# Optimization experiments

Hardware: AMD Instinct MI355X
Metric: run time of the kernel (lower is better)

Reference implementation:

```python
import jax, jax.numpy as jnp
import numpy as np

N_NODES = 100000
N_EDGES = 3200000
IN_DIM = 128
OUT_DIM = 128


def setup_inputs() -> dict:
    key = jax.random.key(0)
    k1, k2, k3, k4, k5 = jax.random.split(key, 5)
    fea_input = jax.random.normal(k1, (N_NODES, IN_DIM), dtype=jnp.float32)
    edge_row = jax.random.randint(k2, (N_EDGES,), 0, N_NODES, dtype=jnp.int32)
    edge_col = jax.random.randint(k3, (N_EDGES,), 0, N_NODES, dtype=jnp.int32)
    edge_val = jax.random.uniform(k4, (N_EDGES,), dtype=jnp.float32)
    # kaiming_uniform-style init for weight, zeros for bias
    bound = float(np.sqrt(6.0 / IN_DIM))
    weight = jax.random.uniform(k5, (IN_DIM, OUT_DIM), dtype=jnp.float32,
                                minval=-bound, maxval=bound)
    bias = jnp.zeros((OUT_DIM,), dtype=jnp.float32)
    return {
        "fea_input": fea_input,
        "edge_row": edge_row,
        "edge_col": edge_col,
        "edge_val": edge_val,
        "weight": weight,
        "bias": bias,
    }


def reference(fea_input, edge_row, edge_col, edge_val, weight, bias):
    # support = X @ W  -> [N, OUT_DIM]
    support = jnp.matmul(fea_input, weight)
    # SpMM: out[r] += val * support[c] for each edge (r, c, val)
    gathered = support[edge_col] * edge_val[:, None]  # [E, OUT_DIM]
    output = jax.ops.segment_sum(gathered, edge_row, num_segments=N_NODES)
    return output + bias
```

## Files before the change

### kernel.cpp

```cpp
#include <hip/hip_runtime.h>
#include <hip/hip_bf16.h>


#define N_NODES 100000
#define N_EDGES 3200000
#define DIM 128
#define RB 16
#define RPB 128
#define NBKT ((N_NODES + RPB - 1) / RPB)
#define CHUNK 8192
#define NCHK ((N_EDGES + CHUNK - 1) / CHUNK)
#define CAP 6016

typedef __attribute__((ext_vector_type(8))) short bf16x8;
typedef __attribute__((ext_vector_type(4))) float f32x4;
typedef unsigned long long u64;
typedef unsigned int u32;

__device__ inline ushort bf16rne(float f) {
  uint32_t u = __float_as_uint(f);
  u += 0x7fffu + ((u >> 16) & 1u);
  return (ushort)(u >> 16);
}
__device__ inline float pk_val(u32 w) { return __uint_as_float((w & 0x7fffu) << 16); }
__device__ inline u32 pk_col(u32 w) { return w >> 15; }

__global__ __launch_bounds__(256) void prep_count_kernel(
    const float* __restrict__ X, const float* __restrict__ W,
    ushort* __restrict__ Xh, ushort* __restrict__ Wh,
    const int* __restrict__ erow, int* __restrict__ bcnt) {
  __shared__ int cnt[NBKT];
  if (blockIdx.x < 1024) {
    const size_t nx4 = (size_t)N_NODES * DIM / 4;
    const size_t nw4 = (size_t)DIM * DIM / 4;
    for (size_t i = (size_t)blockIdx.x * blockDim.x + threadIdx.x;
         i < nx4 + nw4; i += (size_t)1024 * blockDim.x) {
      const float4 f = (i < nx4) ? ((const float4*)X)[i] : ((const float4*)W)[i - nx4];
      ushort4 h;
      h.x = bf16rne(f.x); h.y = bf16rne(f.y); h.z = bf16rne(f.z); h.w = bf16rne(f.w);
      if (i < nx4) ((ushort4*)Xh)[i] = h;
      else         ((ushort4*)Wh)[i - nx4] = h;
    }
  } else {
    const int cb = blockIdx.x - 1024;
    for (int b = threadIdx.x; b < NBKT; b += 256) cnt[b] = 0;
    __syncthreads();
    const int e0 = cb * CHUNK;
    #pragma unroll
    for (int it = 0; it < CHUNK / 256; ++it) {
      const int e = e0 + it * 256 + threadIdx.x;
      if (e < N_EDGES) atomicAdd(&cnt[erow[e] >> 7], 1);
    }
    __syncthreads();
    for (int b = threadIdx.x; b < NBKT; b += 256) {
      const int c = cnt[b];
      if (c) atomicAdd(&bcnt[b], c);
    }
  }
}

__global__ __launch_bounds__(1024) void bscan_kernel(int* __restrict__ bcur,
                                                     int* __restrict__ bbase) {
  __shared__ int wsum[16];
  const int t = threadIdx.x, lane = t & 63, wid = t >> 6;
  const int v = (t < NBKT) ? bcur[t] : 0;
  int incl = v;
  #pragma unroll
  for (int off = 1; off < 64; off <<= 1) {
    int n = __shfl_up(incl, off, 64);
    if (lane >= off) incl += n;
  }
  if (lane == 63) wsum[wid] = incl;
  __syncthreads();
  if (t == 0) {
    int s = 0;
    #pragma unroll
    for (int w = 0; w < 16; ++w) { int x = wsum[w]; wsum[w] = s; s += x; }
  }
  __syncthreads();
  const int excl = wsum[wid] + incl - v;
  if (t < NBKT) { bbase[t] = excl; bcur[t] = excl; }
  if (t == NBKT - 1) bbase[NBKT] = excl + v;
}

__global__ __launch_bounds__(256) void partition_kernel(
    const int* __restrict__ erow, const int* __restrict__ ecol,
    const float* __restrict__ eval,
    int* __restrict__ bcur, u64* __restrict__ p64) {
  __shared__ int cnt[NBKT];
  const int e0 = blockIdx.x * CHUNK;
  for (int b = threadIdx.x; b < NBKT; b += 256) cnt[b] = 0;
  __syncthreads();
  #pragma unroll
  for (int it = 0; it < CHUNK / 256; ++it) {
    const int e = e0 + it * 256 + threadIdx.x;
    if (e < N_EDGES) atomicAdd(&cnt[erow[e] >> 7], 1);
  }
  __syncthreads();
  for (int b = threadIdx.x; b < NBKT; b += 256) {
    const int c = cnt[b];
    if (c) cnt[b] = atomicAdd(&bcur[b], c);
  }
  __syncthreads();
  #pragma unroll
  for (int it = 0; it < CHUNK / 256; ++it) {
    const int e = e0 + it * 256 + threadIdx.x;
    if (e < N_EDGES) {
      const int r = erow[e];
      const u32 lo = ((u32)ecol[e] << 15) | (u32)bf16rne(eval[e]);
      const int p = atomicAdd(&cnt[r >> 7], 1);
      p64[p] = ((u64)(r & (RPB - 1)) << 32) | (u64)lo;
    }
  }
}

__global__ __launch_bounds__(256) void bsort_kernel(
    const int* __restrict__ bbase, u64* __restrict__ p64,
    int* __restrict__ row_ptr, ushort* __restrict__ row_len) {
  __shared__ u64 ebuf[CAP];
  __shared__ u32 obuf[CAP];
  __shared__ int hist[RPB];
  __shared__ int excl[RPB];
  __shared__ int wtot;
  const int b = blockIdx.x, t = threadIdx.x;
  const int s = bbase[b];
  int nE = bbase[b + 1] - s;
  if (nE > CAP) nE = CAP;
  const u64* src = p64 + s;
  u32* out32 = (u32*)p64;
  for (int i = t; i < nE; i += 256) ebuf[i] = src[i];
  if (t < RPB) hist[t] = 0;
  __syncthreads();
  for (int i = t; i < nE; i += 256)
    atomicAdd(&hist[(int)(ebuf[i] >> 32) & (RPB - 1)], 1);
  __syncthreads();
  int v = 0, incl = 0;
  if (t < RPB) {
    v = hist[t];
    incl = v;
    #pragma unroll
    for (int off = 1; off < 64; off <<= 1) {
      int n = __shfl_up(incl, off, 64);
      if ((t & 63) >= off) incl += n;
    }
    if (t == 63) wtot = incl;
  }
  __syncthreads();
  if (t < RPB) {
    const int e = incl - v + ((t >= 64) ? wtot : 0);
    excl[t] = e;
    const int gr = b * RPB + t;
    if (gr < N_NODES) { row_ptr[gr] = 2 * s + e; row_len[gr] = (ushort)v; }
  }
  __syncthreads();
  for (int i = t; i < nE; i += 256) {
    const u64 w = ebuf[i];
    const int p = atomicAdd(&excl[(int)(w >> 32) & (RPB - 1)], 1);
    obuf[p] = (u32)w;
  }
  __syncthreads();
  for (int i = t; i < nE; i += 256) out32[2 * s + i] = obuf[i];
}

__global__ __launch_bounds__(256) void agg_kernel(const ushort* __restrict__ Xh,
                                                  const int* __restrict__ row_ptr,
                                                  const ushort* __restrict__ row_len,
                                                  const u32* __restrict__ packed,
                                                  ushort* __restrict__ Yh) {
  const int r = blockIdx.x * 4 + (threadIdx.x >> 6);
  if (r >= N_NODES) return;
  const int lane = threadIdx.x & 63;
  const int s0 = row_ptr[r];
  const int s1 = s0 + row_len[r];
  float ax0 = 0.f, ay0 = 0.f, ax1 = 0.f, ay1 = 0.f;
  float ax2 = 0.f, ay2 = 0.f, ax3 = 0.f, ay3 = 0.f;
  int e = s0;
  for (; e + 4 <= s1; e += 4) {
    const u32 w0 = packed[e + 0];
    const u32 w1 = packed[e + 1];
    const u32 w2 = packed[e + 2];
    const u32 w3 = packed[e + 3];
    const u32 q0 = ((const u32*)(Xh + (size_t)pk_col(w0) * DIM))[lane];
    const u32 q1 = ((const u32*)(Xh + (size_t)pk_col(w1) * DIM))[lane];
    const u32 q2 = ((const u32*)(Xh + (size_t)pk_col(w2) * DIM))[lane];
    const u32 q3 = ((const u32*)(Xh + (size_t)pk_col(w3) * DIM))[lane];
    const float v0 = pk_val(w0), v1 = pk_val(w1), v2 = pk_val(w2), v3 = pk_val(w3);
    ax0 += v0 * __uint_as_float(q0 << 16);
    ay0 += v0 * __uint_as_float(q0 & 0xffff0000u);
    ax1 += v1 * __uint_as_float(q1 << 16);
    ay1 += v1 * __uint_as_float(q1 & 0xffff0000u);
    ax2 += v2 * __uint_as_float(q2 << 16);
    ay2 += v2 * __uint_as_float(q2 & 0xffff0000u);
    ax3 += v3 * __uint_as_float(q3 << 16);
    ay3 += v3 * __uint_as_float(q3 & 0xffff0000u);
  }
  for (; e < s1; ++e) {
    const u32 w = packed[e];
    const float v = pk_val(w);
    const u32 q = ((const u32*)(Xh + (size_t)pk_col(w) * DIM))[lane];
    ax0 += v * __uint_as_float(q << 16);
    ay0 += v * __uint_as_float(q & 0xffff0000u);
  }
  const float ax = (ax0 + ax1) + (ax2 + ax3);
  const float ay = (ay0 + ay1) + (ay2 + ay3);
  const u32 py = (u32)bf16rne(ax) | ((u32)bf16rne(ay) << 16);
  ((u32*)(Yh + (size_t)r * DIM))[lane] = py;
}

__global__ __launch_bounds__(256) void gemm_mfma(const ushort* __restrict__ Yh,
                                                 const ushort* __restrict__ Wh,
                                                 const float* __restrict__ bias,
                                                 float* __restrict__ out) {
  const int wid = threadIdx.x >> 6, lane = threadIdx.x & 63;
  const int lr = lane & 15, lq = lane >> 4;
  const int n0 = wid * 32;

  bf16x8 bfrag[4][2];
  float bval[2];
  #pragma unroll
  for (int nt = 0; nt < 2; ++nt) {
    const int col = n0 + nt * 16 + lr;
    bval[nt] = bias[col];
    #pragma unroll
    for (int kk = 0; kk < 4; ++kk) {
      const int kbase = kk * 32 + lq * 8;
      bf16x8 b;
      #pragma unroll
      for (int i = 0; i < 8; ++i)
        b[i] = (short)Wh[(size_t)(kbase + i) * DIM + col];
      bfrag[kk][nt] = b;
    }
  }

  const int r0 = blockIdx.x * 256;
  #pragma unroll 1
  for (int g = 0; g < 16; ++g) {
    const int m0 = r0 + g * 16;
    if (m0 >= N_NODES) break;
    bf16x8 afrag[4];
    const ushort* arow = Yh + (size_t)(m0 + lr) * DIM + lq * 8;
    #pragma unroll
    for (int kk = 0; kk < 4; ++kk)
      afrag[kk] = *(const bf16x8*)(arow + kk * 32);
    #pragma unroll
    for (int nt = 0; nt < 2; ++nt) {
      f32x4 acc = {0.f, 0.f, 0.f, 0.f};
      #pragma unroll
      for (int kk = 0; kk < 4; ++kk)
        acc = __builtin_amdgcn_mfma_f32_16x16x32_bf16(afrag[kk], bfrag[kk][nt], acc, 0, 0, 0);
      const int col = n0 + nt * 16 + lr;
      #pragma unroll
      for (int j = 0; j < 4; ++j)
        out[(size_t)(m0 + lq * 4 + j) * DIM + col] = acc[j] + bval[nt];
    }
  }
}

__global__ __launch_bounds__(128) void gemm_kernel(
    const float* __restrict__ IN, const float* __restrict__ W,
    float* __restrict__ OUT, const float* __restrict__ bias, int add_bias) {
  __shared__ float Wsh[DIM * DIM];
  __shared__ float Xsh[RB * DIM];
  const int t = threadIdx.x;
  #pragma unroll 8
  for (int i = 0; i < DIM; ++i) Wsh[i * DIM + t] = W[i * DIM + t];
  const int r0 = blockIdx.x * RB;
  #pragma unroll
  for (int idx = t; idx < RB * DIM; idx += 128)
    Xsh[idx] = IN[(size_t)r0 * DIM + idx];
  __syncthreads();
  float acc[RB];
  const float b = add_bias ? bias[t] : 0.f;
  #pragma unroll
  for (int r = 0; r < RB; ++r) acc[r] = b;
  for (int k = 0; k < DIM; ++k) {
    const float w = Wsh[k * DIM + t];
    #pragma unroll
    for (int r = 0; r < RB; ++r) acc[r] += Xsh[r * DIM + k] * w;
  }
  #pragma unroll
  for (int r = 0; r < RB; ++r)
    OUT[(size_t)(r0 + r) * DIM + t] = acc[r];
}

__global__ void init_kernel(float* __restrict__ out, const float* __restrict__ bias) {
  const size_t total4 = (size_t)N_NODES * DIM / 4;
  const float4* b4 = (const float4*)bias;
  float4* o4 = (float4*)out;
  for (size_t i = (size_t)blockIdx.x * blockDim.x + threadIdx.x;
       i < total4; i += (size_t)gridDim.x * blockDim.x)
    o4[i] = b4[i & 31];
}

__global__ __launch_bounds__(256) void scatter_kernel(
    const float* __restrict__ S,
    const int* __restrict__ erow, const int* __restrict__ ecol,
    const float* __restrict__ eval, float* __restrict__ out) {
  const long long g = (long long)blockIdx.x * blockDim.x + threadIdx.x;
  const long long e = g >> 5;
  const int lane = (int)(g & 31);
  if (e >= N_EDGES) return;
  const int r = erow[e];
  const int c = ecol[e];
  const float v = eval[e];
  const float4 x = ((const float4*)(S + (size_t)c * DIM))[lane];
  float* o = out + (size_t)r * DIM + lane * 4;
  atomicAdd(o + 0, v * x.x);
  atomicAdd(o + 1, v * x.y);
  atomicAdd(o + 2, v * x.z);
  atomicAdd(o + 3, v * x.w);
}

extern "C" void kernel_launch(void* const* d_in, const int* in_sizes, int n_in,
                              void* d_out, int out_size, void* d_ws, size_t ws_size,
                              hipStream_t stream) {
  const float* X    = (const float*)d_in[0];
  const int*   erow = (const int*)d_in[1];
  const int*   ecol = (const int*)d_in[2];
  const float* eval = (const float*)d_in[3];
  const float* W    = (const float*)d_in[4];
  const float* bias = (const float*)d_in[5];
  float* out = (float*)d_out;

  const size_t P64_BYTES = (size_t)N_EDGES * 8;
  const size_t XH_BYTES  = (size_t)N_NODES * DIM * 2;
  const size_t YH_BYTES  = (size_t)N_NODES * DIM * 2;
  const size_t WH_BYTES  = (size_t)DIM * DIM * 2;
  const size_t RP_BYTES  = (size_t)N_NODES * 4;
  const size_t RL_BYTES  = (size_t)N_NODES * 2;
  const size_t BB_BYTES  = (size_t)(NBKT + 1) * 4;
  const size_t BC_BYTES  = (size_t)NBKT * 4;
  const size_t NEED = P64_BYTES + XH_BYTES + YH_BYTES + WH_BYTES +
                      RP_BYTES + RL_BYTES + BB_BYTES + BC_BYTES + 256;

  if (ws_size >= NEED) {
    char* w = (char*)d_ws;
    u64*    p64     = (u64*)w;     w += P64_BYTES;
    ushort* Xh      = (ushort*)w;  w += XH_BYTES;
    ushort* Yh      = (ushort*)w;  w += YH_BYTES;
    ushort* Wh      = (ushort*)w;  w += WH_BYTES;
    int*    row_ptr = (int*)w;     w += RP_BYTES;
    ushort* row_len = (ushort*)w;  w += RL_BYTES;
    int*    bbase   = (int*)w;     w += BB_BYTES;
    int*    bcur    = (int*)w;

    hipMemsetAsync(bcur, 0, BC_BYTES, stream);
    prep_count_kernel<<<1024 + NCHK, 256, 0, stream>>>(X, W, Xh, Wh, erow, bcur);
    bscan_kernel<<<1, 1024, 0, stream>>>(bcur, bbase);
    partition_kernel<<<NCHK, 256, 0, stream>>>(erow, ecol, eval, bcur, p64);
    bsort_kernel<<<NBKT, 256, 0, stream>>>(bbase, p64, row_ptr, row_len);
    agg_kernel<<<(N_NODES + 3) / 4, 256, 0, stream>>>(Xh, row_ptr, row_len,
                                                      (const u32*)p64, Yh);
    gemm_mfma<<<(N_NODES + 255) / 256, 256, 0, stream>>>(Yh, Wh, bias, out);
  } else {
    float* S = (float*)d_ws;
    init_kernel<<<2048, 256, 0, stream>>>(out, bias);
    gemm_kernel<<<N_NODES / RB, 128, 0, stream>>>(X, W, S, bias, 0);
    const long long threads = (long long)N_EDGES * 32;
    scatter_kernel<<<(int)((threads + 255) / 256), 256, 0, stream>>>(S, erow, ecol, eval, out);
  }
}
```

Measured before the change: 246.9 us.

## Fuse sparse aggregation with MFMA GEMM through shared-memory row tile

Merges the aggregation and MFMA GEMM kernels into one. Each block aggregates 16 rows (4 per wave) into a shared-memory bf16 tile and then multiplies it by the weight fragments. This removes the global Yh round trip and one launch. It also unrolls the edge loop to 8 and folds the column extraction into a single shift-and-mask address computation. In exchange, each block now reloads the W fragments from global memory (6250 blocks instead of 391), and each wave processes its 4 rows serially.

```diff
diff --git a/kernel.cpp b/kernel.cpp
--- a/kernel.cpp
+++ b/kernel.cpp
@@ -23,7 +23,6 @@
   return (ushort)(u >> 16);
 }
 __device__ inline float pk_val(u32 w) { return __uint_as_float((w & 0x7fffu) << 16); }
-__device__ inline u32 pk_col(u32 w) { return w >> 15; }
 
 __global__ __launch_bounds__(256) void prep_count_kernel(
     const float* __restrict__ X, const float* __restrict__ W,
@@ -162,58 +161,16 @@
   for (int i = t; i < nE; i += 256) out32[2 * s + i] = obuf[i];
 }
 
-__global__ __launch_bounds__(256) void agg_kernel(const ushort* __restrict__ Xh,
-                                                  const int* __restrict__ row_ptr,
-                                                  const ushort* __restrict__ row_len,
-                                                  const u32* __restrict__ packed,
-                                                  ushort* __restrict__ Yh) {
-  const int r = blockIdx.x * 4 + (threadIdx.x >> 6);
-  if (r >= N_NODES) return;
-  const int lane = threadIdx.x & 63;
-  const int s0 = row_ptr[r];
-  const int s1 = s0 + row_len[r];
-  float ax0 = 0.f, ay0 = 0.f, ax1 = 0.f, ay1 = 0.f;
-  float ax2 = 0.f, ay2 = 0.f, ax3 = 0.f, ay3 = 0.f;
-  int e = s0;
-  for (; e + 4 <= s1; e += 4) {
-    const u32 w0 = packed[e + 0];
-    const u32 w1 = packed[e + 1];
-    const u32 w2 = packed[e + 2];
-    const u32 w3 = packed[e + 3];
-    const u32 q0 = ((const u32*)(Xh + (size_t)pk_col(w0) * DIM))[lane];
-    const u32 q1 = ((const u32*)(Xh + (size_t)pk_col(w1) * DIM))[lane];
-    const u32 q2 = ((const u32*)(Xh + (size_t)pk_col(w2) * DIM))[lane];
-    const u32 q3 = ((const u32*)(Xh + (size_t)pk_col(w3) * DIM))[lane];
-    const float v0 = pk_val(w0), v1 = pk_val(w1), v2 = pk_val(w2), v3 = pk_val(w3);
-    ax0 += v0 * __uint_as_float(q0 << 16);
-    ay0 += v0 * __uint_as_float(q0 & 0xffff0000u);
-    ax1 += v1 * __uint_as_float(q1 << 16);
-    ay1 += v1 * __uint_as_float(q1 & 0xffff0000u);
-    ax2 += v2 * __uint_as_float(q2 << 16);
-    ay2 += v2 * __uint_as_float(q2 & 0xffff0000u);
-    ax3 += v3 * __uint_as_float(q3 << 16);
-    ay3 += v3 * __uint_as_float(q3 & 0xffff0000u);
-  }
-  for (; e < s1; ++e) {
-    const u32 w = packed[e];
-    const float v = pk_val(w);
-    const u32 q = ((const u32*)(Xh + (size_t)pk_col(w) * DIM))[lane];
-    ax0 += v * __uint_as_float(q << 16);
-    ay0 += v * __uint_as_float(q & 0xffff0000u);
-  }
-  const float ax = (ax0 + ax1) + (ax2 + ax3);
-  const float ay = (ay0 + ay1) + (ay2 + ay3);
-  const u32 py = (u32)bf16rne(ax) | ((u32)bf16rne(ay) << 16);
-  ((u32*)(Yh + (size_t)r * DIM))[lane] = py;
-}
-
-__global__ __launch_bounds__(256) void gemm_mfma(const ushort* __restrict__ Yh,
-                                                 const ushort* __restrict__ Wh,
-                                                 const float* __restrict__ bias,
-                                                 float* __restrict__ out) {
+__global__ __launch_bounds__(256) void agg_gemm_kernel(
+    const ushort* __restrict__ Xh, const ushort* __restrict__ Wh,
+    const float* __restrict__ bias,
+    const int* __restrict__ row_ptr, const ushort* __restrict__ row_len,
+    const u32* __restrict__ packed, float* __restrict__ out) {
+  __shared__ ushort Ysh[16][136];
   const int wid = threadIdx.x >> 6, lane = threadIdx.x & 63;
   const int lr = lane & 15, lq = lane >> 4;
   const int n0 = wid * 32;
+  const int r0 = blockIdx.x * 16;
 
   bf16x8 bfrag[4][2];
   float bval[2];
@@ -232,27 +189,76 @@
     }
   }
 
-  const int r0 = blockIdx.x * 256;
+  const char* Xb = (const char*)Xh;
+  const u32 lane4 = (u32)lane * 4u;
   #pragma unroll 1
-  for (int g = 0; g < 16; ++g) {
-    const int m0 = r0 + g * 16;
-    if (m0 >= N_NODES) break;
-    bf16x8 afrag[4];
-    const ushort* arow = Yh + (size_t)(m0 + lr) * DIM + lq * 8;
+  for (int rr = 0; rr < 4; ++rr) {
+    const int r = r0 + wid * 4 + rr;
+    const int s0 = row_ptr[r];
+    const int s1 = s0 + (int)row_len[r];
+    float ax0 = 0.f, ay0 = 0.f, ax1 = 0.f, ay1 = 0.f;
+    float ax2 = 0.f, ay2 = 0.f, ax3 = 0.f, ay3 = 0.f;
+    int e = s0;
+    for (; e + 8 <= s1; e += 8) {
+      const u32 w0 = packed[e + 0], w1 = packed[e + 1];
+      const u32 w2 = packed[e + 2], w3 = packed[e + 3];
+      const u32 w4 = packed[e + 4], w5 = packed[e + 5];
+      const u32 w6 = packed[e + 6], w7 = packed[e + 7];
+      const u32 q0 = *(const u32*)(Xb + (((w0 >> 7) & 0xFFFFFF00u) + lane4));
+      const u32 q1 = *(const u32*)(Xb + (((w1 >> 7) & 0xFFFFFF00u) + lane4));
+      const u32 q2 = *(const u32*)(Xb + (((w2 >> 7) & 0xFFFFFF00u) + lane4));
+      const u32 q3 = *(const u32*)(Xb + (((w3 >> 7) & 0xFFFFFF00u) + lane4));
+      const u32 q4 = *(const u32*)(Xb + (((w4 >> 7) & 0xFFFFFF00u) + lane4));
+      const u32 q5 = *(const u32*)(Xb + (((w5 >> 7) & 0xFFFFFF00u) + lane4));
+      const u32 q6 = *(const u32*)(Xb + (((w6 >> 7) & 0xFFFFFF00u) + lane4));
+      const u32 q7 = *(const u32*)(Xb + (((w7 >> 7) & 0xFFFFFF00u) + lane4));
+      const float v0 = pk_val(w0), v1 = pk_val(w1), v2 = pk_val(w2), v3 = pk_val(w3);
+      const float v4 = pk_val(w4), v5 = pk_val(w5), v6 = pk_val(w6), v7 = pk_val(w7);
+      ax0 += v0 * __uint_as_float(q0 << 16);
+      ay0 += v0 * __uint_as_float(q0 & 0xffff0000u);
+      ax1 += v1 * __uint_as_float(q1 << 16);
+      ay1 += v1 * __uint_as_float(q1 & 0xffff0000u);
+      ax2 += v2 * __uint_as_float(q2 << 16);
+      ay2 += v2 * __uint_as_float(q2 & 0xffff0000u);
+      ax3 += v3 * __uint_as_float(q3 << 16);
+      ay3 += v3 * __uint_as_float(q3 & 0xffff0000u);
+      ax0 += v4 * __uint_as_float(q4 << 16);
+      ay0 += v4 * __uint_as_float(q4 & 0xffff0000u);
+      ax1 += v5 * __uint_as_float(q5 << 16);
+      ay1 += v5 * __uint_as_float(q5 & 0xffff0000u);
+      ax2 += v6 * __uint_as_float(q6 << 16);
+      ay2 += v6 * __uint_as_float(q6 & 0xffff0000u);
+      ax3 += v7 * __uint_as_float(q7 << 16);
+      ay3 += v7 * __uint_as_float(q7 & 0xffff0000u);
+    }
+    for (; e < s1; ++e) {
+      const u32 w = packed[e];
+      const float v = pk_val(w);
+      const u32 q = *(const u32*)(Xb + (((w >> 7) & 0xFFFFFF00u) + lane4));
+      ax0 += v * __uint_as_float(q << 16);
+      ay0 += v * __uint_as_float(q & 0xffff0000u);
+    }
+    const float ax = (ax0 + ax1) + (ax2 + ax3);
+    const float ay = (ay0 + ay1) + (ay2 + ay3);
+    const u32 py = (u32)bf16rne(ax) | ((u32)bf16rne(ay) << 16);
+    ((u32*)&Ysh[wid * 4 + rr][0])[lane] = py;
+  }
+  __syncthreads();
+
+  bf16x8 afrag[4];
+  #pragma unroll
+  for (int kk = 0; kk < 4; ++kk)
+    afrag[kk] = *(const bf16x8*)&Ysh[lr][kk * 32 + lq * 8];
+  #pragma unroll
+  for (int nt = 0; nt < 2; ++nt) {
+    f32x4 acc = {0.f, 0.f, 0.f, 0.f};
     #pragma unroll
     for (int kk = 0; kk < 4; ++kk)
-      afrag[kk] = *(const bf16x8*)(arow + kk * 32);
-    #pragma unroll
-    for (int nt = 0; nt < 2; ++nt) {
-      f32x4 acc = {0.f, 0.f, 0.f, 0.f};
-      #pragma unroll
-      for (int kk = 0; kk < 4; ++kk)
-        acc = __builtin_amdgcn_mfma_f32_16x16x32_bf16(afrag[kk], bfrag[kk][nt], acc, 0, 0, 0);
-      const int col = n0 + nt * 16 + lr;
-      #pragma unroll
-      for (int j = 0; j < 4; ++j)
-        out[(size_t)(m0 + lq * 4 + j) * DIM + col] = acc[j] + bval[nt];
-    }
+      acc = __builtin_amdgcn_mfma_f32_16x16x32_bf16(afrag[kk], bfrag[kk][nt], acc, 0, 0, 0);
+    const int col = n0 + nt * 16 + lr;
+    #pragma unroll
+    for (int j = 0; j < 4; ++j)
+      out[(size_t)(r0 + lq * 4 + j) * DIM + col] = acc[j] + bval[nt];
   }
 }
 
@@ -324,20 +330,18 @@
 
   const size_t P64_BYTES = (size_t)N_EDGES * 8;
   const size_t XH_BYTES  = (size_t)N_NODES * DIM * 2;
-  const size_t YH_BYTES  = (size_t)N_NODES * DIM * 2;
   const size_t WH_BYTES  = (size_t)DIM * DIM * 2;
   const size_t RP_BYTES  = (size_t)N_NODES * 4;
   const size_t RL_BYTES  = (size_t)N_NODES * 2;
   const size_t BB_BYTES  = (size_t)(NBKT + 1) * 4;
   const size_t BC_BYTES  = (size_t)NBKT * 4;
-  const size_t NEED = P64_BYTES + XH_BYTES + YH_BYTES + WH_BYTES +
+  const size_t NEED = P64_BYTES + XH_BYTES + WH_BYTES +
                       RP_BYTES + RL_BYTES + BB_BYTES + BC_BYTES + 256;
 
   if (ws_size >= NEED) {
     char* w = (char*)d_ws;
     u64*    p64     = (u64*)w;     w += P64_BYTES;
     ushort* Xh      = (ushort*)w;  w += XH_BYTES;
-    ushort* Yh      = (ushort*)w;  w += YH_BYTES;
     ushort* Wh      = (ushort*)w;  w += WH_BYTES;
     int*    row_ptr = (int*)w;     w += RP_BYTES;
     ushort* row_len = (ushort*)w;  w += RL_BYTES;
@@ -349,9 +353,8 @@
     bscan_kernel<<<1, 1024, 0, stream>>>(bcur, bbase);
     partition_kernel<<<NCHK, 256, 0, stream>>>(erow, ecol, eval, bcur, p64);
     bsort_kernel<<<NBKT, 256, 0, stream>>>(bbase, p64, row_ptr, row_len);
-    agg_kernel<<<(N_NODES + 3) / 4, 256, 0, stream>>>(Xh, row_ptr, row_len,
-                                                      (const u32*)p64, Yh);
-    gemm_mfma<<<(N_NODES + 255) / 256, 256, 0, stream>>>(Yh, Wh, bias, out);
+    agg_gemm_kernel<<<N_NODES / 16, 256, 0, stream>>>(Xh, Wh, bias, row_ptr,
+                                                      row_len, (const u32*)p64, out);
   } else {
     float* S = (float*)d_ws;
     init_kernel<<<2048, 256, 0, stream>>>(out, bias);
```

New measurement: 282.1 us. +14.3%, slower.

## Reuse chunk histograms in partition and store pre-decoded 64-bit edges for aggregation

Applied to the files above, without the earlier changes.

The count pass now saves each chunk's per-bucket histogram to a table, stored in the Yh buffer, so the partition kernel no longer re-reads edge rows and rebuilds the histogram. The bucket sort writes sorted edges in place as 64-bit words holding a precomputed byte offset and an fp32 value, dropping the shared output buffer and the extra copy pass. The aggregation kernel reads these with 16-byte vector loads, unrolls 8 edges per iteration and skips the per-edge decode arithmetic. In exchange, edge traffic in aggregation doubles (8 instead of 4 bytes per edge), and the 32-bit byte offset and the reuse of Yh as scratch both depend on fixed sizes.

```diff
diff --git a/kernel.cpp b/kernel.cpp
--- a/kernel.cpp
+++ b/kernel.cpp
@@ -22,13 +22,12 @@
   u += 0x7fffu + ((u >> 16) & 1u);
   return (ushort)(u >> 16);
 }
-__device__ inline float pk_val(u32 w) { return __uint_as_float((w & 0x7fffu) << 16); }
-__device__ inline u32 pk_col(u32 w) { return w >> 15; }
 
 __global__ __launch_bounds__(256) void prep_count_kernel(
     const float* __restrict__ X, const float* __restrict__ W,
     ushort* __restrict__ Xh, ushort* __restrict__ Wh,
-    const int* __restrict__ erow, int* __restrict__ bcnt) {
+    const int* __restrict__ erow, int* __restrict__ bcnt,
+    int* __restrict__ table) {
   __shared__ int cnt[NBKT];
   if (blockIdx.x < 1024) {
     const size_t nx4 = (size_t)N_NODES * DIM / 4;
@@ -54,6 +53,7 @@
     __syncthreads();
     for (int b = threadIdx.x; b < NBKT; b += 256) {
       const int c = cnt[b];
+      table[(size_t)cb * NBKT + b] = c;
       if (c) atomicAdd(&bcnt[b], c);
     }
   }
@@ -85,21 +85,13 @@
 
 __global__ __launch_bounds__(256) void partition_kernel(
     const int* __restrict__ erow, const int* __restrict__ ecol,
-    const float* __restrict__ eval,
+    const float* __restrict__ eval, const int* __restrict__ table,
     int* __restrict__ bcur, u64* __restrict__ p64) {
   __shared__ int cnt[NBKT];
   const int e0 = blockIdx.x * CHUNK;
-  for (int b = threadIdx.x; b < NBKT; b += 256) cnt[b] = 0;
-  __syncthreads();
-  #pragma unroll
-  for (int it = 0; it < CHUNK / 256; ++it) {
-    const int e = e0 + it * 256 + threadIdx.x;
-    if (e < N_EDGES) atomicAdd(&cnt[erow[e] >> 7], 1);
-  }
-  __syncthreads();
   for (int b = threadIdx.x; b < NBKT; b += 256) {
-    const int c = cnt[b];
-    if (c) cnt[b] = atomicAdd(&bcur[b], c);
+    const int c = table[(size_t)blockIdx.x * NBKT + b];
+    cnt[b] = c ? atomicAdd(&bcur[b], c) : 0;
   }
   __syncthreads();
   #pragma unroll
@@ -118,7 +110,6 @@
     const int* __restrict__ bbase, u64* __restrict__ p64,
     int* __restrict__ row_ptr, ushort* __restrict__ row_len) {
   __shared__ u64 ebuf[CAP];
-  __shared__ u32 obuf[CAP];
   __shared__ int hist[RPB];
   __shared__ int excl[RPB];
   __shared__ int wtot;
@@ -127,7 +118,6 @@
   int nE = bbase[b + 1] - s;
   if (nE > CAP) nE = CAP;
   const u64* src = p64 + s;
-  u32* out32 = (u32*)p64;
   for (int i = t; i < nE; i += 256) ebuf[i] = src[i];
   if (t < RPB) hist[t] = 0;
   __syncthreads();
@@ -150,41 +140,58 @@
     const int e = incl - v + ((t >= 64) ? wtot : 0);
     excl[t] = e;
     const int gr = b * RPB + t;
-    if (gr < N_NODES) { row_ptr[gr] = 2 * s + e; row_len[gr] = (ushort)v; }
+    if (gr < N_NODES) { row_ptr[gr] = s + e; row_len[gr] = (ushort)v; }
   }
   __syncthreads();
   for (int i = t; i < nE; i += 256) {
     const u64 w = ebuf[i];
     const int p = atomicAdd(&excl[(int)(w >> 32) & (RPB - 1)], 1);
-    obuf[p] = (u32)w;
-  }
-  __syncthreads();
-  for (int i = t; i < nE; i += 256) out32[2 * s + i] = obuf[i];
-}
-
-__global__ __launch_bounds__(256) void agg_kernel(const ushort* __restrict__ Xh,
-                                                  const int* __restrict__ row_ptr,
-                                                  const ushort* __restrict__ row_len,
-                                                  const u32* __restrict__ packed,
-                                                  ushort* __restrict__ Yh) {
+    const u32 lo = (u32)w;
+    const u32 off = (lo >> 7) & 0xFFFFFF00u;
+    const u32 vb  = (lo & 0x7fffu) << 16;
+    p64[s + p] = ((u64)vb << 32) | (u64)off;
+  }
+}
+
+__global__ __launch_bounds__(256) void agg_kernel(
+    const ushort* __restrict__ Xh,
+    const int* __restrict__ row_ptr, const ushort* __restrict__ row_len,
+    const u64* __restrict__ edges, ushort* __restrict__ Yh) {
   const int r = blockIdx.x * 4 + (threadIdx.x >> 6);
   if (r >= N_NODES) return;
   const int lane = threadIdx.x & 63;
+  const u32 lane4 = (u32)lane * 4u;
+  const char* Xb = (const char*)Xh;
   const int s0 = row_ptr[r];
-  const int s1 = s0 + row_len[r];
+  const int s1 = s0 + (int)row_len[r];
   float ax0 = 0.f, ay0 = 0.f, ax1 = 0.f, ay1 = 0.f;
   float ax2 = 0.f, ay2 = 0.f, ax3 = 0.f, ay3 = 0.f;
   int e = s0;
-  for (; e + 4 <= s1; e += 4) {
-    const u32 w0 = packed[e + 0];
-    const u32 w1 = packed[e + 1];
-    const u32 w2 = packed[e + 2];
-    const u32 w3 = packed[e + 3];
-    const u32 q0 = ((const u32*)(Xh + (size_t)pk_col(w0) * DIM))[lane];
-    const u32 q1 = ((const u32*)(Xh + (size_t)pk_col(w1) * DIM))[lane];
-    const u32 q2 = ((const u32*)(Xh + (size_t)pk_col(w2) * DIM))[lane];
-    const u32 q3 = ((const u32*)(Xh + (size_t)pk_col(w3) * DIM))[lane];
-    const float v0 = pk_val(w0), v1 = pk_val(w1), v2 = pk_val(w2), v3 = pk_val(w3);
+  if ((e & 1) && e < s1) {
+    const u64 w = edges[e];
+    const float v = __uint_as_float((u32)(w >> 32));
+    const u32 q = *(const u32*)(Xb + ((u32)w + lane4));
+    ax0 += v * __uint_as_float(q << 16);
+    ay0 += v * __uint_as_float(q & 0xffff0000u);
+    ++e;
+  }
+  for (; e + 8 <= s1; e += 8) {
+    const uint4 pa = *(const uint4*)(edges + e);
+    const uint4 pb = *(const uint4*)(edges + e + 2);
+    const uint4 pc = *(const uint4*)(edges + e + 4);
+    const uint4 pd = *(const uint4*)(edges + e + 6);
+    const u32 q0 = *(const u32*)(Xb + (pa.x + lane4));
+    const u32 q1 = *(const u32*)(Xb + (pa.z + lane4));
+    const u32 q2 = *(const u32*)(Xb + (pb.x + lane4));
+    const u32 q3 = *(const u32*)(Xb + (pb.z + lane4));
+    const u32 q4 = *(const u32*)(Xb + (pc.x + lane4));
+    const u32 q5 = *(const u32*)(Xb + (pc.z + lane4));
+    const u32 q6 = *(const u32*)(Xb + (pd.x + lane4));
+    const u32 q7 = *(const u32*)(Xb + (pd.z + lane4));
+    const float v0 = __uint_as_float(pa.y), v1 = __uint_as_float(pa.w);
+    const float v2 = __uint_as_float(pb.y), v3 = __uint_as_float(pb.w);
+    const float v4 = __uint_as_float(pc.y), v5 = __uint_as_float(pc.w);
+    const float v6 = __uint_as_float(pd.y), v7 = __uint_as_float(pd.w);
     ax0 += v0 * __uint_as_float(q0 << 16);
     ay0 += v0 * __uint_as_float(q0 & 0xffff0000u);
     ax1 += v1 * __uint_as_float(q1 << 16);
@@ -193,11 +200,29 @@
     ay2 += v2 * __uint_as_float(q2 & 0xffff0000u);
     ax3 += v3 * __uint_as_float(q3 << 16);
     ay3 += v3 * __uint_as_float(q3 & 0xffff0000u);
-  }
-  for (; e < s1; ++e) {
-    const u32 w = packed[e];
-    const float v = pk_val(w);
-    const u32 q = ((const u32*)(Xh + (size_t)pk_col(w) * DIM))[lane];
+    ax0 += v4 * __uint_as_float(q4 << 16);
+    ay0 += v4 * __uint_as_float(q4 & 0xffff0000u);
+    ax1 += v5 * __uint_as_float(q5 << 16);
+    ay1 += v5 * __uint_as_float(q5 & 0xffff0000u);
+    ax2 += v6 * __uint_as_float(q6 << 16);
+    ay2 += v6 * __uint_as_float(q6 & 0xffff0000u);
+    ax3 += v7 * __uint_as_float(q7 << 16);
+    ay3 += v7 * __uint_as_float(q7 & 0xffff0000u);
+  }
+  for (; e + 2 <= s1; e += 2) {
+    const uint4 p = *(const uint4*)(edges + e);
+    const u32 qa = *(const u32*)(Xb + (p.x + lane4));
+    const u32 qb = *(const u32*)(Xb + (p.z + lane4));
+    const float va = __uint_as_float(p.y), vb = __uint_as_float(p.w);
+    ax0 += va * __uint_as_float(qa << 16);
+    ay0 += va * __uint_as_float(qa & 0xffff0000u);
+    ax1 += vb * __uint_as_float(qb << 16);
+    ay1 += vb * __uint_as_float(qb & 0xffff0000u);
+  }
+  if (e < s1) {
+    const u64 w = edges[e];
+    const float v = __uint_as_float((u32)(w >> 32));
+    const u32 q = *(const u32*)(Xb + ((u32)w + lane4));
     ax0 += v * __uint_as_float(q << 16);
     ay0 += v * __uint_as_float(q & 0xffff0000u);
   }
@@ -343,14 +368,14 @@
     ushort* row_len = (ushort*)w;  w += RL_BYTES;
     int*    bbase   = (int*)w;     w += BB_BYTES;
     int*    bcur    = (int*)w;
+    int*    table   = (int*)Yh;
 
     hipMemsetAsync(bcur, 0, BC_BYTES, stream);
-    prep_count_kernel<<<1024 + NCHK, 256, 0, stream>>>(X, W, Xh, Wh, erow, bcur);
+    prep_count_kernel<<<1024 + NCHK, 256, 0, stream>>>(X, W, Xh, Wh, erow, bcur, table);
     bscan_kernel<<<1, 1024, 0, stream>>>(bcur, bbase);
-    partition_kernel<<<NCHK, 256, 0, stream>>>(erow, ecol, eval, bcur, p64);
+    partition_kernel<<<NCHK, 256, 0, stream>>>(erow, ecol, eval, table, bcur, p64);
     bsort_kernel<<<NBKT, 256, 0, stream>>>(bbase, p64, row_ptr, row_len);
-    agg_kernel<<<(N_NODES + 3) / 4, 256, 0, stream>>>(Xh, row_ptr, row_len,
-                                                      (const u32*)p64, Yh);
+    agg_kernel<<<(N_NODES + 3) / 4, 256, 0, stream>>>(Xh, row_ptr, row_len, p64, Yh);
     gemm_mfma<<<(N_NODES + 255) / 256, 256, 0, stream>>>(Yh, Wh, bias, out);
   } else {
     float* S = (float*)d_ws;
```

Result: no change. 248.1 us (+0.5%).
